# Kernel optimization log

Measured on AMD Instinct MI355X. Metric: run time of the kernel, lower is better.

Reference implementation:

```python
import jax, jax.numpy as jnp
import numpy as np
from jax import lax

EPS = 1e-5  # torch BatchNorm default eps

# Binarization with straight-through estimator (hard-tanh gradient window),
# matching BinaryFunc in dizcza/MCMC_BinaryNet.
@jax.custom_vjp
def binarize(x):
    return jnp.sign(x)

def _bin_fwd(x):
    return jnp.sign(x), x

def _bin_bwd(res, g):
    return (g * (jnp.abs(res) <= 1.0).astype(g.dtype),)

binarize.defvjp(_bin_fwd, _bin_bwd)

def bn2d(x, gamma, beta):
    # training-mode BatchNorm2d: batch stats over (N,H,W), biased variance
    m = x.mean(axis=(0, 2, 3), keepdims=True)
    v = x.var(axis=(0, 2, 3), keepdims=True)
    xn = (x - m) * lax.rsqrt(v + EPS)
    return xn * gamma[None, :, None, None] + beta[None, :, None, None]

def bn1d(x, gamma, beta):
    m = x.mean(axis=0, keepdims=True)
    v = x.var(axis=0, keepdims=True)
    return (x - m) * lax.rsqrt(v + EPS) * gamma[None, :] + beta[None, :]

def bconv(x, w):
    # BinaryDecorator(Conv2d): sign(x) conv sign(W), padding=0, no bias
    return lax.conv_general_dilated(binarize(x), binarize(w), (1, 1), 'VALID',
                                    dimension_numbers=('NCHW', 'OIHW', 'NCHW'))

def maxpool2(x):
    return lax.reduce_window(x, -jnp.inf, lax.max, (1, 1, 2, 2), (1, 1, 2, 2), 'VALID')

def prelu(x, a):
    return jnp.where(x >= 0, x, a * x)


def setup_inputs() -> dict:
    key = jax.random.key(0)
    ks = iter(jax.random.split(key, 16))
    conv_channels = [3, 128, 256, 512]
    fc_sizes = [512 * 6 * 6, 1024, 10]
    d = {'x': jax.random.normal(next(ks), (128, 3, 64, 64), jnp.float32)}
    for i, (cin, cout) in enumerate(zip(conv_channels[:-1], conv_channels[1:])):
        d[f'cg{i}'] = jnp.ones((cin,), jnp.float32)          # BN2d gamma
        d[f'cb{i}'] = jnp.zeros((cin,), jnp.float32)         # BN2d beta
        d[f'cw{i}'] = jax.random.normal(next(ks), (cout, cin, 3, 3), jnp.float32) * 0.05
        d[f'cp{i}'] = jnp.full((1,), 0.25, jnp.float32)      # PReLU (num_parameters=1)
    for i, (fin, fout) in enumerate(zip(fc_sizes[:-1], fc_sizes[1:])):
        d[f'fg{i}'] = jnp.ones((fin,), jnp.float32)
        d[f'fb{i}'] = jnp.zeros((fin,), jnp.float32)
        d[f'fw{i}'] = jax.random.normal(next(ks), (fout, fin), jnp.float32) * 0.05
        d[f'fp{i}'] = jnp.full((1,), 0.25, jnp.float32)
    d['scale'] = jnp.full((1,), 1e-3, jnp.float32)           # ScaleLayer init
    return d


def reference(x, cg0, cb0, cw0, cp0, cg1, cb1, cw1, cp1, cg2, cb2, cw2, cp2,
              fg0, fb0, fw0, fp0, fg1, fb1, fw1, fp1, scale):
    for cg, cb, cw, cp in ((cg0, cb0, cw0, cp0), (cg1, cb1, cw1, cp1), (cg2, cb2, cw2, cp2)):
        x = bn2d(x, cg, cb)
        x = bconv(x, cw)
        x = maxpool2(x)
        x = prelu(x, cp)
    x = x.reshape(x.shape[0], -1)  # [B, 512*6*6]
    for fg, fb, fw, fp in ((fg0, fb0, fw0, fp0), (fg1, fb1, fw1, fp1)):
        x = bn1d(x, fg, fb)
        x = binarize(x) @ binarize(fw).T  # BinaryDecorator(Linear), no bias
        x = prelu(x, fp)
    return x * scale
```

## Files before the change

### kernel.cpp

```cpp
#include <hip/hip_runtime.h>
#include <cstdint>
#include <cstddef>

#define BN_EPS 1e-5


__global__ void zero_d(double* p, int n) {
  int i = blockIdx.x * blockDim.x + threadIdx.x;
  if (i < n) p[i] = 0.0;
}

__global__ void reduce_plane_p(const float* __restrict__ x, double* __restrict__ pp,
                               int C, int HW) {
  int c = blockIdx.x, n = blockIdx.y;
  const float* p = x + ((long)n * C + c) * HW;
  double s = 0.0, s2 = 0.0;
  for (int i = threadIdx.x; i < HW; i += blockDim.x) {
    double v = (double)p[i];
    s += v; s2 += v * v;
  }
  for (int o = 32; o > 0; o >>= 1) {
    s  += __shfl_down(s, o, 64);
    s2 += __shfl_down(s2, o, 64);
  }
  __shared__ double ls[4], ls2[4];
  int lane = threadIdx.x & 63, w = threadIdx.x >> 6;
  if (lane == 0) { ls[w] = s; ls2[w] = s2; }
  __syncthreads();
  if (threadIdx.x == 0) {
    double a = 0, b = 0;
    for (int i = 0; i < 4; i++) { a += ls[i]; b += ls2[i]; }
    long o = ((long)n * C + c) * 2;
    pp[o] = a; pp[o + 1] = b;
  }
}

__global__ void finalize_plane_par(const double* __restrict__ pp, double2* __restrict__ st,
                                   int C, int N, double cnt) {
  int c = blockIdx.x;
  double s = 0.0, s2 = 0.0;
  for (int n = threadIdx.x; n < N; n += blockDim.x) {
    long o = ((long)n * C + c) * 2;
    s  += pp[o];
    s2 += pp[o + 1];
  }
  for (int o = 32; o > 0; o >>= 1) {
    s  += __shfl_down(s, o, 64);
    s2 += __shfl_down(s2, o, 64);
  }
  __shared__ double ls[2], ls2[2];
  int lane = threadIdx.x & 63, w = threadIdx.x >> 6;
  if (lane == 0) { ls[w] = s; ls2[w] = s2; }
  __syncthreads();
  if (threadIdx.x == 0) {
    double a = ls[0] + ls[1], b = ls2[0] + ls2[1];
    double m = a / cnt;
    double v = b / cnt - m * m;
    st[c] = make_double2(m, 1.0 / sqrt(v + BN_EPS));
  }
}

__global__ void finalize_pp1(const double2* __restrict__ pp, double2* __restrict__ st,
                             int C, int Y, double cnt) {
  int c = blockIdx.x;
  double s = 0.0, s2 = 0.0;
  for (int y = threadIdx.x; y < Y; y += blockDim.x) {
    double2 p = pp[(long)y * C + c];
    s += p.x; s2 += p.y;
  }
  for (int o = 32; o > 0; o >>= 1) {
    s  += __shfl_down(s, o, 64);
    s2 += __shfl_down(s2, o, 64);
  }
  __shared__ double ls[4], ls2[4];
  int lane = threadIdx.x & 63, w = threadIdx.x >> 6;
  if (lane == 0) { ls[w] = s; ls2[w] = s2; }
  __syncthreads();
  if (threadIdx.x == 0) {
    double a = ls[0] + ls[1] + ls[2] + ls[3];
    double b = ls2[0] + ls2[1] + ls2[2] + ls2[3];
    double m = a / cnt;
    double v = b / cnt - m * m;
    st[c] = make_double2(m, 1.0 / sqrt(v + BN_EPS));
  }
}

__global__ void finalize_pp2(const double2* __restrict__ pp, double2* __restrict__ st,
                             double cnt) {
  int c = blockIdx.x;
  int cg = c >> 6, l = c & 63;
  double s = 0.0, s2 = 0.0;
  for (int y = threadIdx.x; y < 512; y += blockDim.x) {
    int n = y >> 2, ch = y & 3;
    double2 p = pp[(long)(n * 16 + cg * 4 + ch) * 64 + l];
    s += p.x; s2 += p.y;
  }
  for (int o = 32; o > 0; o >>= 1) {
    s  += __shfl_down(s, o, 64);
    s2 += __shfl_down(s2, o, 64);
  }
  __shared__ double ls[4], ls2[4];
  int lane = threadIdx.x & 63, w = threadIdx.x >> 6;
  if (lane == 0) { ls[w] = s; ls2[w] = s2; }
  __syncthreads();
  if (threadIdx.x == 0) {
    double a = ls[0] + ls[1] + ls[2] + ls[3];
    double b = ls2[0] + ls2[1] + ls2[2] + ls2[3];
    double m = a / cnt;
    double v = b / cnt - m * m;
    st[c] = make_double2(m, 1.0 / sqrt(v + BN_EPS));
  }
}

__global__ void reduce_cols2_i16(const short* __restrict__ x, const float* __restrict__ cp,
                                 double* __restrict__ sums, int R, int F, int RS) {
  int f = blockIdx.x * blockDim.x + threadIdx.x;
  int r0 = blockIdx.y * RS, r1 = min(r0 + RS, R);
  float alpha = cp[0];
  double s = 0.0, s2 = 0.0;
  for (int r = r0; r < r1; r++) {
    int xi = x[(long)r * F + f];
    float pr = xi >= 0 ? (float)xi : alpha * (float)xi;
    double v = (double)pr;
    s += v; s2 += v * v;
  }
  atomicAdd(&sums[2 * f], s);
  atomicAdd(&sums[2 * f + 1], s2);
}

__global__ void reduce_cols2(const float* __restrict__ x, double* __restrict__ sums,
                             int R, int F, int RS) {
  int f = blockIdx.x * blockDim.x + threadIdx.x;
  int r0 = blockIdx.y * RS, r1 = min(r0 + RS, R);
  double s = 0.0, s2 = 0.0;
  for (int r = r0; r < r1; r++) {
    double v = (double)x[(long)r * F + f];
    s += v; s2 += v * v;
  }
  atomicAdd(&sums[2 * f], s);
  atomicAdd(&sums[2 * f + 1], s2);
}

__global__ void finalize_stats(const double* __restrict__ sums, double2* __restrict__ st,
                               int C, double cnt) {
  int c = blockIdx.x * blockDim.x + threadIdx.x;
  if (c >= C) return;
  double m = sums[2 * c] / cnt;
  double v = sums[2 * c + 1] / cnt - m * m;
  st[c] = make_double2(m, 1.0 / sqrt(v + BN_EPS));
}


__global__ void pack_bits_c1(const float* __restrict__ x, const double2* __restrict__ st,
                             const float* __restrict__ g, const float* __restrict__ b,
                             uint64_t* __restrict__ rows, int nwid) {
  long base = ((long)blockIdx.x * 4 + (threadIdx.x >> 6)) * 8;
  int lane = threadIdx.x & 63;
  for (int j = 0; j < 8; j++) {
    long wid = base + j;
    if (wid >= nwid) return;
    int n = (int)(wid / 192), rem = (int)(wid % 192);
    int ci = rem >> 6, y = rem & 63;
    double2 s = st[ci];
    float xv = x[(((long)n * 3 + ci) * 64 + y) * 64 + lane];
    float xn = (float)(((double)xv - s.x) * s.y) * g[ci] + b[ci];
    uint64_t m = __ballot(xn > 0.f);
    if (lane == 0) rows[wid] = m;
  }
}

__global__ void pack_wc1(const float* __restrict__ w, uint32_t* __restrict__ wm) {
  int co = threadIdx.x;
  uint32_t m = 0;
  for (int j = 0; j < 27; j++) m |= (uint32_t)(w[co * 27 + j] > 0.f) << j;
  wm[co] = m;
}

__global__ void pack_cl_i8(const signed char* __restrict__ acl, const double2* __restrict__ st,
                           const float* __restrict__ g, const float* __restrict__ b,
                           const float* __restrict__ cp, uint64_t* __restrict__ out,
                           int C, long nwords, int lw) {
  long base = ((long)blockIdx.x * 4 + (threadIdx.x >> 6)) * 8;
  int lane = threadIdx.x & 63;
  float alpha = cp[0];
  for (int j = 0; j < 8; j++) {
    long wid = base + j;
    if (wid >= nwords) return;
    long row = wid >> lw;
    int w = (int)(wid & ((1 << lw) - 1));
    int c = w * 64 + lane;
    double2 s = st[c];
    int xi = acl[row * C + c];
    float pr = xi >= 0 ? (float)xi : alpha * (float)xi;
    float xn = (float)(((double)pr - s.x) * s.y) * g[c] + b[c];
    uint64_t m = __ballot(xn > 0.f);
    if (lane == 0) out[wid] = m;
  }
}

__global__ void pack_cl_i16(const short* __restrict__ acl, const double2* __restrict__ st,
                            const float* __restrict__ g, const float* __restrict__ b,
                            const float* __restrict__ cp, uint64_t* __restrict__ out,
                            int C, long nwords, int lw) {
  long base = ((long)blockIdx.x * 4 + (threadIdx.x >> 6)) * 8;
  int lane = threadIdx.x & 63;
  float alpha = cp[0];
  for (int j = 0; j < 8; j++) {
    long wid = base + j;
    if (wid >= nwords) return;
    long row = wid >> lw;
    int w = (int)(wid & ((1 << lw) - 1));
    int c = w * 64 + lane;
    double2 s = st[c];
    int xi = acl[row * C + c];
    float pr = xi >= 0 ? (float)xi : alpha * (float)xi;
    float xn = (float)(((double)pr - s.x) * s.y) * g[c] + b[c];
    uint64_t m = __ballot(xn > 0.f);
    if (lane == 0) out[wid] = m;
  }
}

__global__ void pack_wconv(const float* __restrict__ w, uint64_t* __restrict__ out,
                           int CO, int CI, int W) {
  int i = blockIdx.x * blockDim.x + threadIdx.x;
  int total = CO * 9 * W;
  if (i >= total) return;
  int wd = i % W;
  int t = i / W;
  int tap = t % 9, co = t / 9;
  uint64_t bits = 0;
  for (int k = 0; k < 64; k++) {
    int ci = wd * 64 + k;
    bits |= (uint64_t)(w[((long)co * CI + ci) * 9 + tap] > 0.f) << k;
  }
  out[i] = bits;
}

__global__ void pack_nz_i16(const short* __restrict__ x, const double2* __restrict__ st,
                            const float* __restrict__ g, const float* __restrict__ b,
                            const float* __restrict__ cp, uint64_t* __restrict__ out,
                            int R, int F) {
  int Wf = F >> 6;
  long base = ((long)blockIdx.x * 4 + (threadIdx.x >> 6)) * 8;
  int lane = threadIdx.x & 63;
  float alpha = cp[0];
  for (int j = 0; j < 8; j++) {
    long wid = base + j;
    if (wid >= (long)R * Wf) return;
    long r = wid / Wf;
    int w = (int)(wid % Wf);
    int f = w * 64 + lane;
    double2 s = st[f];
    int xi = x[r * F + f];
    float pr = xi >= 0 ? (float)xi : alpha * (float)xi;
    double d = (double)pr - s.x;
    float xn = (float)(d * s.y) * g[f] + b[f];
    uint64_t sm = __ballot(xn > 0.f);
    uint64_t nm = __ballot(d != 0.0);
    if (lane == 0) { out[2 * wid] = sm; out[2 * wid + 1] = nm; }
  }
}

__global__ void pack_nz(const float* __restrict__ x, const double2* __restrict__ st,
                        const float* __restrict__ g, const float* __restrict__ b,
                        uint64_t* __restrict__ out, int R, int F) {
  int Wf = F >> 6;
  long base = ((long)blockIdx.x * 4 + (threadIdx.x >> 6)) * 8;
  int lane = threadIdx.x & 63;
  for (int j = 0; j < 8; j++) {
    long wid = base + j;
    if (wid >= (long)R * Wf) return;
    long r = wid / Wf;
    int w = (int)(wid % Wf);
    int f = w * 64 + lane;
    double2 s = st[f];
    double d = (double)x[r * F + f] - s.x;
    float xn = (float)(d * s.y) * g[f] + b[f];
    uint64_t sm = __ballot(xn > 0.f);
    uint64_t nm = __ballot(d != 0.0);
    if (lane == 0) { out[2 * wid] = sm; out[2 * wid + 1] = nm; }
  }
}

__global__ void pack_wfc2_t(const float* __restrict__ w, uint64_t* __restrict__ out,
                            int O, int F) {
  int Wf = F >> 6;
  long base = ((long)blockIdx.x * 4 + (threadIdx.x >> 6)) * 8;
  int lane = threadIdx.x & 63;
  for (int j = 0; j < 8; j++) {
    long wid = base + j;
    if (wid >= (long)O * Wf) return;
    long o = wid / Wf;
    int wd = (int)(wid % Wf);
    uint64_t m = __ballot(w[o * F + wd * 64 + lane] > 0.f);
    if (lane == 0) out[(long)wd * O + o] = m;
  }
}


__global__ __launch_bounds__(256) void conv1_pool3_i8(const uint64_t* __restrict__ rows,
                                                      const uint32_t* __restrict__ wm,
                                                      const float* __restrict__ cp,
                                                      signed char* __restrict__ out,
                                                      double2* __restrict__ pp) {
  __shared__ uint64_t rL[192];
  __shared__ uint32_t wL[128];
  __shared__ uint32_t mL[61 * 4];
  __shared__ double2 sm[256];
  int n = blockIdx.y, chunk = blockIdx.x, t = threadIdx.x;
  if (t < 192) rL[t] = rows[n * 192 + t];
  if (t < 128) wL[t] = wm[t];
  __syncthreads();
  if (t < 244) {
    int pl = t >> 2, quad = t & 3;
    int pos = chunk * 61 + pl;
    if (pos < 961) {
      int py = pos / 31, px = pos - py * 31;
      int cy = 2 * py + (quad >> 1), cx = 2 * px + (quad & 1);
      uint32_t m = 0;
#pragma unroll
      for (int ci = 0; ci < 3; ci++)
#pragma unroll
        for (int ky = 0; ky < 3; ky++)
          m |= (uint32_t)((rL[ci * 64 + cy + ky] >> cx) & 7) << (ci * 9 + ky * 3);
      mL[pl * 4 + quad] = m;
    }
  }
  __syncthreads();
  int co = t & 127, slot = t >> 7;
  float alpha = cp[0];
  uint32_t w = wL[co];
  double s = 0.0, s2 = 0.0;
  for (int i = slot; i < 61; i += 2) {
    int pos = chunk * 61 + i;
    if (pos >= 961) break;
    int p0 = __popc(mL[4 * i] ^ w);
    int p1 = __popc(mL[4 * i + 1] ^ w);
    int p2 = __popc(mL[4 * i + 2] ^ w);
    int p3 = __popc(mL[4 * i + 3] ^ w);
    int dot = 27 - 2 * min(min(p0, p1), min(p2, p3));
    out[((long)n * 961 + pos) * 128 + co] = (signed char)dot;
    float pr = dot >= 0 ? (float)dot : alpha * (float)dot;
    double v = (double)pr;
    s += v; s2 += v * v;
  }
  sm[t] = make_double2(s, s2);
  __syncthreads();
  if (t < 128) {
    double2 a = sm[t], b = sm[t + 128];
    pp[((long)n * 16 + chunk) * 128 + t] = make_double2(a.x + b.x, a.y + b.y);
  }
}

template <int W, int IH, int PH, int CHUNK>
__global__ __attribute__((amdgpu_flat_work_group_size(256, 256),
                          amdgpu_waves_per_eu(3, 4)))
void convp_carry_i16(const uint64_t* __restrict__ in, const uint64_t* __restrict__ wt,
                     const float* __restrict__ cp, short* __restrict__ out,
                     double2* __restrict__ pp, int CO) {
  __shared__ uint64_t sIn[10 * IH * W];
  __shared__ double2 sm[256];
  int n = blockIdx.y;
  int cg = blockIdx.x / CHUNK, chunk = blockIdx.x % CHUNK;
  int t = threadIdx.x, lane = t & 63, slot = t >> 6;
  int r0 = chunk * 8;
  int nr = min(10, IH - r0);
  const uint64_t* src = in + ((long)n * IH + r0) * (IH * W);
  for (int i = t; i < nr * IH * W; i += 256) sIn[i] = src[i];
  int co = cg * 64 + lane;
  uint64_t wr[9 * W];
  const uint64_t* wg = wt + (long)co * (9 * W);
#pragma unroll
  for (int i = 0; i < 9 * W; i++) wr[i] = wg[i];
  __syncthreads();
  int py = chunk * 4 + slot;
  float alpha = cp[0];
  double s = 0.0, s2 = 0.0;
  if (py < PH) {
    const int K = 9 * 64 * W;
    const uint64_t* base = &sIn[(2 * slot) * (IH * W)];
    uint64_t c[4][2 * W];
#pragma unroll
    for (int cy = 0; cy < 4; cy++) {
      const uint64_t* p = &base[(cy * IH) * W];
#pragma unroll
      for (int j = 0; j < 2 * W; j++) c[cy][j] = p[j];
    }
#pragma unroll
    for (int px = 0; px < PH; px++) {
      int a00 = 0, a01 = 0, a10 = 0, a11 = 0;
#pragma unroll
      for (int cy = 0; cy < 4; cy++) {
        uint64_t f[2 * W];
        const uint64_t* fp = &base[(cy * IH + 2 * px + 2) * W];
#pragma unroll
        for (int j = 0; j < 2 * W; j++) f[j] = fp[j];
#pragma unroll
        for (int col = 0; col < 4; col++) {
#pragma unroll
          for (int wd = 0; wd < W; wd++) {
            uint64_t v = (col < 2) ? c[cy][col * W + wd] : f[(col - 2) * W + wd];
#pragma unroll
            for (int dy = 0; dy < 2; dy++) {
              int ky = cy - dy;
              if (ky < 0 || ky > 2) continue;
#pragma unroll
              for (int dx = 0; dx < 2; dx++) {
                int kx = col - dx;
                if (kx < 0 || kx > 2) continue;
                int p = __popcll(v ^ wr[(ky * 3 + kx) * W + wd]);
                if (dy == 0) { if (dx == 0) a00 += p; else a01 += p; }
                else         { if (dx == 0) a10 += p; else a11 += p; }
              }
            }
          }
        }
#pragma unroll
        for (int j = 0; j < 2 * W; j++) c[cy][j] = f[j];
      }
      int dot = K - 2 * min(min(a00, a01), min(a10, a11));
      out[((long)n * PH * PH + py * PH + px) * CO + co] = (short)dot;
      float pr = dot >= 0 ? (float)dot : alpha * (float)dot;
      double v = (double)pr;
      s += v; s2 += v * v;
    }
  }
  sm[t] = make_double2(s, s2);
  __syncthreads();
  if (t < 64) {
    double2 a = sm[t], b = sm[64 + t], cc = sm[128 + t], d = sm[192 + t];
    pp[((long)blockIdx.y * 16 + blockIdx.x) * 64 + t] =
        make_double2(a.x + b.x + cc.x + d.x, a.y + b.y + cc.y + d.y);
  }
}

#define TAP2(acc, P, wa, wb) acc += __popcll((P).x ^ (wa)) + __popcll((P).y ^ (wb));
#define ROWT(aL, aR, pA, pB, pC, pD, WX, WY, WZ)                \
  TAP2(aL, pA, WX.x, WX.y) TAP2(aL, pB, WY.x, WY.y)             \
  TAP2(aL, pC, WZ.x, WZ.y)                                      \
  TAP2(aR, pB, WX.x, WX.y) TAP2(aR, pC, WY.x, WY.y)             \
  TAP2(aR, pD, WZ.x, WZ.y)

__global__ __attribute__((amdgpu_flat_work_group_size(256, 256),
                          amdgpu_waves_per_eu(4, 6)))
void convs3_i16(const uint64_t* __restrict__ in, const uint64_t* __restrict__ wt,
                short* __restrict__ out) {
  __shared__ uint64_t sIn[14 * 14 * 4];
  int n = blockIdx.y, cg = blockIdx.x;
  int t = threadIdx.x, lane = t & 63, slot = t >> 6;
  const uint64_t* src = in + (long)n * 784;
  for (int i = t; i < 784; i += 256) sIn[i] = src[i];
  int h = lane >> 5;
  int co = cg * 32 + (lane & 31);
  const uint64_t* wg = wt + co * 36 + 2 * h;
  ulonglong2 W0 = *(const ulonglong2*)(wg + 0);
  ulonglong2 W1 = *(const ulonglong2*)(wg + 4);
  ulonglong2 W2 = *(const ulonglong2*)(wg + 8);
  ulonglong2 W3 = *(const ulonglong2*)(wg + 12);
  ulonglong2 W4 = *(const ulonglong2*)(wg + 16);
  ulonglong2 W5 = *(const ulonglong2*)(wg + 20);
  ulonglong2 W6 = *(const ulonglong2*)(wg + 24);
  ulonglong2 W7 = *(const ulonglong2*)(wg + 28);
  ulonglong2 W8 = *(const ulonglong2*)(wg + 32);
  __syncthreads();
  short* outb = out + ((long)n * 512 + co) * 36;
#pragma unroll
  for (int k = 0; k < 9; k++) {
    int pos = slot + 4 * k;
    int py = pos / 6, px = pos - py * 6;
    const uint64_t* q = sIn + ((2 * py) * 14 + 2 * px) * 4 + 2 * h;
    int a00 = 0, a01 = 0, a10 = 0, a11 = 0;
    {
      ulonglong2 p0 = *(const ulonglong2*)(q + 0);
      ulonglong2 p1 = *(const ulonglong2*)(q + 4);
      ulonglong2 p2 = *(const ulonglong2*)(q + 8);
      ulonglong2 p3 = *(const ulonglong2*)(q + 12);
      ROWT(a00, a01, p0, p1, p2, p3, W0, W1, W2)
    }
    {
      const uint64_t* q1 = q + 56;
      ulonglong2 p0 = *(const ulonglong2*)(q1 + 0);
      ulonglong2 p1 = *(const ulonglong2*)(q1 + 4);
      ulonglong2 p2 = *(const ulonglong2*)(q1 + 8);
      ulonglong2 p3 = *(const ulonglong2*)(q1 + 12);
      ROWT(a00, a01, p0, p1, p2, p3, W3, W4, W5)
      ROWT(a10, a11, p0, p1, p2, p3, W0, W1, W2)
    }
    {
      const uint64_t* q2 = q + 112;
      ulonglong2 p0 = *(const ulonglong2*)(q2 + 0);
      ulonglong2 p1 = *(const ulonglong2*)(q2 + 4);
      ulonglong2 p2 = *(const ulonglong2*)(q2 + 8);
      ulonglong2 p3 = *(const ulonglong2*)(q2 + 12);
      ROWT(a00, a01, p0, p1, p2, p3, W6, W7, W8)
      ROWT(a10, a11, p0, p1, p2, p3, W3, W4, W5)
    }
    {
      const uint64_t* q3 = q + 168;
      ulonglong2 p0 = *(const ulonglong2*)(q3 + 0);
      ulonglong2 p1 = *(const ulonglong2*)(q3 + 4);
      ulonglong2 p2 = *(const ulonglong2*)(q3 + 8);
      ulonglong2 p3 = *(const ulonglong2*)(q3 + 12);
      ROWT(a10, a11, p0, p1, p2, p3, W6, W7, W8)
    }
    int t00 = a00 + __shfl_xor(a00, 32);
    int t01 = a01 + __shfl_xor(a01, 32);
    int t10 = a10 + __shfl_xor(a10, 32);
    int t11 = a11 + __shfl_xor(a11, 32);
    if (h == 0) {
      int dot = 2304 - 2 * min(min(t00, t01), min(t10, t11));
      outb[pos] = (short)dot;
    }
  }
}


__global__ void fc_bin2(const uint64_t* __restrict__ xp, const uint64_t* __restrict__ wp_t,
                        const float* __restrict__ cp, float* __restrict__ out,
                        int O, int Wf) {
  __shared__ uint64_t xs[2][288], xz[2][288];
  int r0 = blockIdx.y * 2;
  for (int i = threadIdx.x; i < 2 * Wf; i += blockDim.x) {
    int rr = i / Wf, wd = i - rr * Wf;
    xs[rr][wd] = xp[(((long)(r0 + rr)) * Wf + wd) * 2];
    xz[rr][wd] = xp[(((long)(r0 + rr)) * Wf + wd) * 2 + 1];
  }
  __syncthreads();
  int o = blockIdx.x * blockDim.x + threadIdx.x;
  if (o >= O) return;
  int pc0 = 0, pc1 = 0, nz0 = 0, nz1 = 0;
  for (int wd = 0; wd < Wf; wd++) {
    uint64_t w = wp_t[(long)wd * O + o];
    uint64_t z0 = xz[0][wd], z1 = xz[1][wd];
    pc0 += __popcll((xs[0][wd] ^ w) & z0);
    pc1 += __popcll((xs[1][wd] ^ w) & z1);
    nz0 += __popcll(z0);
    nz1 += __popcll(z1);
  }
  float alpha = cp[0];
  int d0 = nz0 - 2 * pc0, d1 = nz1 - 2 * pc1;
  float f0 = (float)d0, f1 = (float)d1;
  out[(long)r0 * O + o] = d0 >= 0 ? f0 : alpha * f0;
  out[(long)(r0 + 1) * O + o] = d1 >= 0 ? f1 : alpha * f1;
}

__global__ void fc_bin_scale(const uint64_t* __restrict__ xp, const uint64_t* __restrict__ wp_t,
                             const float* __restrict__ cp, const float* __restrict__ scale,
                             float* __restrict__ out, int R, int O, int Wf) {
  int i = blockIdx.x * blockDim.x + threadIdx.x;
  if (i >= R * O) return;
  int o = i % O, r = i / O;
  int pc = 0, nzc = 0;
  for (int wd = 0; wd < Wf; wd++) {
    uint64_t nz = xp[((long)r * Wf + wd) * 2 + 1];
    pc += __popcll((xp[((long)r * Wf + wd) * 2] ^ wp_t[(long)wd * O + o]) & nz);
    nzc += __popcll(nz);
  }
  int dot = nzc - 2 * pc;
  float f = (float)dot;
  float alpha = cp[0];
  f = dot >= 0 ? f : alpha * f;
  out[i] = f * scale[0];
}


extern "C" void kernel_launch(void* const* d_in, const int* in_sizes, int n_in,
                              void* d_out, int out_size, void* d_ws, size_t ws_size,
                              hipStream_t stream) {
  const float* x   = (const float*)d_in[0];
  const float* cg0 = (const float*)d_in[1];
  const float* cb0 = (const float*)d_in[2];
  const float* cw0 = (const float*)d_in[3];
  const float* cp0 = (const float*)d_in[4];
  const float* cg1 = (const float*)d_in[5];
  const float* cb1 = (const float*)d_in[6];
  const float* cw1 = (const float*)d_in[7];
  const float* cp1 = (const float*)d_in[8];
  const float* cg2 = (const float*)d_in[9];
  const float* cb2 = (const float*)d_in[10];
  const float* cw2 = (const float*)d_in[11];
  const float* cp2 = (const float*)d_in[12];
  const float* fg0 = (const float*)d_in[13];
  const float* fb0 = (const float*)d_in[14];
  const float* fw0 = (const float*)d_in[15];
  const float* fp0 = (const float*)d_in[16];
  const float* fg1 = (const float*)d_in[17];
  const float* fb1 = (const float*)d_in[18];
  const float* fw1 = (const float*)d_in[19];
  const float* fp1 = (const float*)d_in[20];
  const float* scl = (const float*)d_in[21];

  char* ws = (char*)d_ws;
  size_t off = 0;
  auto alloc = [&](size_t bytes) {
    size_t r = off;
    off += (bytes + 255) & ~(size_t)255;
    return r;
  };
  const int C0_OFF = 0, C1_OFF = 16, C2_OFF = 160, C3_OFF = 448, C4_OFF = 18944;
  const int NCH = 19968;

  double*   sums  = (double*)(ws + alloc((size_t)NCH * 2 * sizeof(double)));
  double2*  stats = (double2*)(ws + alloc((size_t)NCH * sizeof(double2)));
  double*   pplane= (double*)(ws + alloc(128L * 3 * 2 * sizeof(double)));
  double2*  pp1   = (double2*)(ws + alloc(2048L * 128 * sizeof(double2)));
  double2*  pp2   = (double2*)(ws + alloc(2048L * 64 * sizeof(double2)));
  uint64_t* rows0 = (uint64_t*)(ws + alloc(128L * 3 * 64 * 8));
  uint32_t* wm1   = (uint32_t*)(ws + alloc(128L * 4));
  signed char* a1 = (signed char*)(ws + alloc(128L * 961 * 128));
  uint64_t* s1p   = (uint64_t*)(ws + alloc(128L * 961 * 2 * 8));
  uint64_t* w1p   = (uint64_t*)(ws + alloc(256L * 9 * 2 * 8));
  short*    a2    = (short*)(ws + alloc(128L * 196 * 256 * 2));
  uint64_t* s2p   = (uint64_t*)(ws + alloc(128L * 196 * 4 * 8));
  uint64_t* w2p   = (uint64_t*)(ws + alloc(512L * 9 * 4 * 8));
  short*    a3    = (short*)(ws + alloc(128L * 512 * 36 * 2));
  uint64_t* s3p   = (uint64_t*)(ws + alloc(128L * 288 * 2 * 8));
  uint64_t* w3p   = (uint64_t*)(ws + alloc(1024L * 288 * 8));
  float*    f1    = (float*)(ws + alloc(128L * 1024 * 4));
  uint64_t* s4p   = (uint64_t*)(ws + alloc(128L * 16 * 2 * 8));
  uint64_t* w4p   = (uint64_t*)(ws + alloc(10L * 16 * 8));

  const int B = 256;

  zero_d<<<dim3(153), B, 0, stream>>>(sums + 2 * C3_OFF, (NCH - C3_OFF) * 2);

  reduce_plane_p<<<dim3(3, 128), B, 0, stream>>>(x, pplane, 3, 4096);
  finalize_plane_par<<<dim3(3), 128, 0, stream>>>(pplane, stats + C0_OFF, 3, 128, 524288.0);
  pack_bits_c1<<<dim3(768), B, 0, stream>>>(x, stats + C0_OFF, cg0, cb0, rows0, 24576);
  pack_wc1<<<1, 128, 0, stream>>>(cw0, wm1);
  conv1_pool3_i8<<<dim3(16, 128), B, 0, stream>>>(rows0, wm1, cp0, a1, pp1);

  finalize_pp1<<<dim3(128), B, 0, stream>>>(pp1, stats + C1_OFF, 128, 2048, 123008.0);
  pack_cl_i8<<<dim3(7688), B, 0, stream>>>(a1, stats + C1_OFF, cg1, cb1, cp0, s1p, 128, 246016L, 1);
  pack_wconv<<<dim3(18), B, 0, stream>>>(cw1, w1p, 256, 128, 2);
  convp_carry_i16<2, 31, 14, 4><<<dim3(16, 128), B, 0, stream>>>(s1p, w1p, cp1, a2, pp2, 256);

  finalize_pp2<<<dim3(256), B, 0, stream>>>(pp2, stats + C2_OFF, 25088.0);
  pack_cl_i16<<<dim3(3136), B, 0, stream>>>(a2, stats + C2_OFF, cg2, cb2, cp1, s2p, 256, 100352L, 2);
  pack_wconv<<<dim3(72), B, 0, stream>>>(cw2, w2p, 512, 256, 4);
  convs3_i16<<<dim3(16, 128), B, 0, stream>>>(s2p, w2p, a3);

  reduce_cols2_i16<<<dim3(72, 8), B, 0, stream>>>(a3, cp2, sums + 2 * C3_OFF, 128, 18432, 16);
  finalize_stats<<<dim3(72), B, 0, stream>>>(sums + 2 * C3_OFF, stats + C3_OFF, 18432, 128.0);
  pack_nz_i16<<<dim3(1152), B, 0, stream>>>(a3, stats + C3_OFF, fg0, fb0, cp2, s3p, 128, 18432);
  pack_wfc2_t<<<dim3(9216), B, 0, stream>>>(fw0, w3p, 1024, 18432);
  fc_bin2<<<dim3(4, 64), B, 0, stream>>>(s3p, w3p, fp0, f1, 1024, 288);

  reduce_cols2<<<dim3(4, 8), B, 0, stream>>>(f1, sums + 2 * C4_OFF, 128, 1024, 16);
  finalize_stats<<<dim3(4), B, 0, stream>>>(sums + 2 * C4_OFF, stats + C4_OFF, 1024, 128.0);
  pack_nz<<<dim3(64), B, 0, stream>>>(f1, stats + C4_OFF, fg1, fb1, s4p, 128, 1024);
  pack_wfc2_t<<<dim3(5), B, 0, stream>>>(fw1, w4p, 10, 1024);
  fc_bin_scale<<<dim3(5), B, 0, stream>>>(s4p, w4p, fp1, scl, (float*)d_out, 128, 10, 16);
}
```

Baseline: 494.7 us.

## Merge weight packing into one launch and fuse BN stat finalization into consumers

All weight-binarization kernels and the zeroing of the sums buffer are merged into a single multi-role launch. The BN statistic finalize kernels are folded into the packing kernels that consume them: layer-0 stats are computed in shared memory inside pack_bits_c1, and FC0 stats are computed on the fly from the sums. The FC0 GEMM now emits per-row-pair partial sums, so the last BN, pack and FC1 run in one fused per-row kernel. This removes about ten kernel launches and their serialization gaps, at the cost of redundant per-block stat recomputation.

```diff
diff --git a/kernel.cpp b/kernel.cpp
--- a/kernel.cpp
+++ b/kernel.cpp
@@ -5,9 +5,61 @@
 #define BN_EPS 1e-5
 
 
-__global__ void zero_d(double* p, int n) {
-  int i = blockIdx.x * blockDim.x + threadIdx.x;
-  if (i < n) p[i] = 0.0;
+__global__ void pack_weights_all(const float* __restrict__ cw0, const float* __restrict__ cw1,
+                                 const float* __restrict__ cw2, const float* __restrict__ fw0,
+                                 const float* __restrict__ fw1,
+                                 uint32_t* __restrict__ wm1, uint64_t* __restrict__ w1p,
+                                 uint64_t* __restrict__ w2p, uint64_t* __restrict__ w3p,
+                                 uint64_t* __restrict__ w4p, double* __restrict__ zp, int zn) {
+  int bb = blockIdx.x, t = threadIdx.x, lane = t & 63, wv = t >> 6;
+  if (bb == 0) {
+    if (t < 128) {
+      uint32_t m = 0;
+      for (int j = 0; j < 27; j++) m |= (uint32_t)(cw0[t * 27 + j] > 0.f) << j;
+      wm1[t] = m;
+    }
+  } else if (bb < 19) {
+    int i = (bb - 1) * 256 + t;
+    if (i < 4608) {
+      int wd = i % 2, t2 = i / 2, tap = t2 % 9, co = t2 / 9;
+      uint64_t bits = 0;
+      for (int k = 0; k < 64; k++)
+        bits |= (uint64_t)(cw1[((long)co * 128 + wd * 64 + k) * 9 + tap] > 0.f) << k;
+      w1p[i] = bits;
+    }
+  } else if (bb < 91) {
+    int i = (bb - 19) * 256 + t;
+    if (i < 18432) {
+      int wd = i % 4, t2 = i / 4, tap = t2 % 9, co = t2 / 9;
+      uint64_t bits = 0;
+      for (int k = 0; k < 64; k++)
+        bits |= (uint64_t)(cw2[((long)co * 256 + wd * 64 + k) * 9 + tap] > 0.f) << k;
+      w2p[i] = bits;
+    }
+  } else if (bb < 9307) {
+    long base = ((long)(bb - 91) * 4 + wv) * 8;
+    for (int j = 0; j < 8; j++) {
+      long wid = base + j;
+      if (wid >= 294912) break;
+      long o = wid / 288;
+      int wd = (int)(wid % 288);
+      uint64_t m = __ballot(fw0[o * 18432 + wd * 64 + lane] > 0.f);
+      if (lane == 0) w3p[(long)wd * 1024 + o] = m;
+    }
+  } else if (bb < 9312) {
+    long base = ((long)(bb - 9307) * 4 + wv) * 8;
+    for (int j = 0; j < 8; j++) {
+      long wid = base + j;
+      if (wid >= 160) break;
+      long o = wid / 16;
+      int wd = (int)(wid % 16);
+      uint64_t m = __ballot(fw1[o * 1024 + wd * 64 + lane] > 0.f);
+      if (lane == 0) w4p[(long)wd * 10 + o] = m;
+    }
+  } else {
+    int i = (bb - 9312) * 256 + t;
+    if (i < zn) zp[i] = 0.0;
+  }
 }
 
 __global__ void reduce_plane_p(const float* __restrict__ x, double* __restrict__ pp,
@@ -35,28 +87,37 @@
   }
 }
 
-__global__ void finalize_plane_par(const double* __restrict__ pp, double2* __restrict__ st,
-                                   int C, int N, double cnt) {
-  int c = blockIdx.x;
-  double s = 0.0, s2 = 0.0;
-  for (int n = threadIdx.x; n < N; n += blockDim.x) {
-    long o = ((long)n * C + c) * 2;
-    s  += pp[o];
-    s2 += pp[o + 1];
-  }
-  for (int o = 32; o > 0; o >>= 1) {
-    s  += __shfl_down(s, o, 64);
-    s2 += __shfl_down(s2, o, 64);
-  }
-  __shared__ double ls[2], ls2[2];
-  int lane = threadIdx.x & 63, w = threadIdx.x >> 6;
-  if (lane == 0) { ls[w] = s; ls2[w] = s2; }
-  __syncthreads();
-  if (threadIdx.x == 0) {
-    double a = ls[0] + ls[1], b = ls2[0] + ls2[1];
-    double m = a / cnt;
-    double v = b / cnt - m * m;
-    st[c] = make_double2(m, 1.0 / sqrt(v + BN_EPS));
+__global__ void pack_bits_c1_f(const float* __restrict__ x, const double* __restrict__ pplane,
+                               const float* __restrict__ g, const float* __restrict__ b,
+                               uint64_t* __restrict__ rows, int nwid) {
+  __shared__ double2 stc[3];
+  int t = threadIdx.x, lane = t & 63, wv = t >> 6;
+  if (wv < 3) {
+    int c = wv;
+    double s  = pplane[((long)lane * 3 + c) * 2]     + pplane[((long)(lane + 64) * 3 + c) * 2];
+    double s2 = pplane[((long)lane * 3 + c) * 2 + 1] + pplane[((long)(lane + 64) * 3 + c) * 2 + 1];
+    for (int o = 32; o > 0; o >>= 1) {
+      s  += __shfl_down(s, o, 64);
+      s2 += __shfl_down(s2, o, 64);
+    }
+    if (lane == 0) {
+      double m = s / 524288.0;
+      double v = s2 / 524288.0 - m * m;
+      stc[c] = make_double2(m, 1.0 / sqrt(v + BN_EPS));
+    }
+  }
+  __syncthreads();
+  long base = ((long)blockIdx.x * 4 + wv) * 8;
+  for (int j = 0; j < 8; j++) {
+    long wid = base + j;
+    if (wid >= nwid) return;
+    int n = (int)(wid / 192), rem = (int)(wid % 192);
+    int ci = rem >> 6, y = rem & 63;
+    double2 s = stc[ci];
+    float xv = x[(((long)n * 3 + ci) * 64 + y) * 64 + lane];
+    float xn = (float)(((double)xv - s.x) * s.y) * g[ci] + b[ci];
+    uint64_t m = __ballot(xn > 0.f);
+    if (lane == 0) rows[wid] = m;
   }
 }
 
@@ -128,53 +189,6 @@
   atomicAdd(&sums[2 * f + 1], s2);
 }
 
-__global__ void reduce_cols2(const float* __restrict__ x, double* __restrict__ sums,
-                             int R, int F, int RS) {
-  int f = blockIdx.x * blockDim.x + threadIdx.x;
-  int r0 = blockIdx.y * RS, r1 = min(r0 + RS, R);
-  double s = 0.0, s2 = 0.0;
-  for (int r = r0; r < r1; r++) {
-    double v = (double)x[(long)r * F + f];
-    s += v; s2 += v * v;
-  }
-  atomicAdd(&sums[2 * f], s);
-  atomicAdd(&sums[2 * f + 1], s2);
-}
-
-__global__ void finalize_stats(const double* __restrict__ sums, double2* __restrict__ st,
-                               int C, double cnt) {
-  int c = blockIdx.x * blockDim.x + threadIdx.x;
-  if (c >= C) return;
-  double m = sums[2 * c] / cnt;
-  double v = sums[2 * c + 1] / cnt - m * m;
-  st[c] = make_double2(m, 1.0 / sqrt(v + BN_EPS));
-}
-
-
-__global__ void pack_bits_c1(const float* __restrict__ x, const double2* __restrict__ st,
-                             const float* __restrict__ g, const float* __restrict__ b,
-                             uint64_t* __restrict__ rows, int nwid) {
-  long base = ((long)blockIdx.x * 4 + (threadIdx.x >> 6)) * 8;
-  int lane = threadIdx.x & 63;
-  for (int j = 0; j < 8; j++) {
-    long wid = base + j;
-    if (wid >= nwid) return;
-    int n = (int)(wid / 192), rem = (int)(wid % 192);
-    int ci = rem >> 6, y = rem & 63;
-    double2 s = st[ci];
-    float xv = x[(((long)n * 3 + ci) * 64 + y) * 64 + lane];
-    float xn = (float)(((double)xv - s.x) * s.y) * g[ci] + b[ci];
-    uint64_t m = __ballot(xn > 0.f);
-    if (lane == 0) rows[wid] = m;
-  }
-}
-
-__global__ void pack_wc1(const float* __restrict__ w, uint32_t* __restrict__ wm) {
-  int co = threadIdx.x;
-  uint32_t m = 0;
-  for (int j = 0; j < 27; j++) m |= (uint32_t)(w[co * 27 + j] > 0.f) << j;
-  wm[co] = m;
-}
 
 __global__ void pack_cl_i8(const signed char* __restrict__ acl, const double2* __restrict__ st,
                            const float* __restrict__ g, const float* __restrict__ b,
@@ -220,26 +234,10 @@
   }
 }
 
-__global__ void pack_wconv(const float* __restrict__ w, uint64_t* __restrict__ out,
-                           int CO, int CI, int W) {
-  int i = blockIdx.x * blockDim.x + threadIdx.x;
-  int total = CO * 9 * W;
-  if (i >= total) return;
-  int wd = i % W;
-  int t = i / W;
-  int tap = t % 9, co = t / 9;
-  uint64_t bits = 0;
-  for (int k = 0; k < 64; k++) {
-    int ci = wd * 64 + k;
-    bits |= (uint64_t)(w[((long)co * CI + ci) * 9 + tap] > 0.f) << k;
-  }
-  out[i] = bits;
-}
-
-__global__ void pack_nz_i16(const short* __restrict__ x, const double2* __restrict__ st,
-                            const float* __restrict__ g, const float* __restrict__ b,
-                            const float* __restrict__ cp, uint64_t* __restrict__ out,
-                            int R, int F) {
+__global__ void pack_nz_st_i16(const short* __restrict__ x, const double* __restrict__ sums,
+                               const float* __restrict__ g, const float* __restrict__ b,
+                               const float* __restrict__ cp, uint64_t* __restrict__ out,
+                               int R, int F) {
   int Wf = F >> 6;
   long base = ((long)blockIdx.x * 4 + (threadIdx.x >> 6)) * 8;
   int lane = threadIdx.x & 63;
@@ -250,50 +248,16 @@
     long r = wid / Wf;
     int w = (int)(wid % Wf);
     int f = w * 64 + lane;
-    double2 s = st[f];
+    double m = sums[2 * f] / 128.0;
+    double v = sums[2 * f + 1] / 128.0 - m * m;
+    double rs = 1.0 / sqrt(v + BN_EPS);
     int xi = x[r * F + f];
     float pr = xi >= 0 ? (float)xi : alpha * (float)xi;
-    double d = (double)pr - s.x;
-    float xn = (float)(d * s.y) * g[f] + b[f];
+    double d = (double)pr - m;
+    float xn = (float)(d * rs) * g[f] + b[f];
     uint64_t sm = __ballot(xn > 0.f);
     uint64_t nm = __ballot(d != 0.0);
     if (lane == 0) { out[2 * wid] = sm; out[2 * wid + 1] = nm; }
-  }
-}
-
-__global__ void pack_nz(const float* __restrict__ x, const double2* __restrict__ st,
-                        const float* __restrict__ g, const float* __restrict__ b,
-                        uint64_t* __restrict__ out, int R, int F) {
-  int Wf = F >> 6;
-  long base = ((long)blockIdx.x * 4 + (threadIdx.x >> 6)) * 8;
-  int lane = threadIdx.x & 63;
-  for (int j = 0; j < 8; j++) {
-    long wid = base + j;
-    if (wid >= (long)R * Wf) return;
-    long r = wid / Wf;
-    int w = (int)(wid % Wf);
-    int f = w * 64 + lane;
-    double2 s = st[f];
-    double d = (double)x[r * F + f] - s.x;
-    float xn = (float)(d * s.y) * g[f] + b[f];
-    uint64_t sm = __ballot(xn > 0.f);
-    uint64_t nm = __ballot(d != 0.0);
-    if (lane == 0) { out[2 * wid] = sm; out[2 * wid + 1] = nm; }
-  }
-}
-
-__global__ void pack_wfc2_t(const float* __restrict__ w, uint64_t* __restrict__ out,
-                            int O, int F) {
-  int Wf = F >> 6;
-  long base = ((long)blockIdx.x * 4 + (threadIdx.x >> 6)) * 8;
-  int lane = threadIdx.x & 63;
-  for (int j = 0; j < 8; j++) {
-    long wid = base + j;
-    if (wid >= (long)O * Wf) return;
-    long o = wid / Wf;
-    int wd = (int)(wid % Wf);
-    uint64_t m = __ballot(w[o * F + wd * 64 + lane] > 0.f);
-    if (lane == 0) out[(long)wd * O + o] = m;
   }
 }
 
@@ -515,9 +479,9 @@
 }
 
 
-__global__ void fc_bin2(const uint64_t* __restrict__ xp, const uint64_t* __restrict__ wp_t,
-                        const float* __restrict__ cp, float* __restrict__ out,
-                        int O, int Wf) {
+__global__ void fc_bin2_pp(const uint64_t* __restrict__ xp, const uint64_t* __restrict__ wp_t,
+                           const float* __restrict__ cp, float* __restrict__ out,
+                           double2* __restrict__ pp3, int O, int Wf) {
   __shared__ uint64_t xs[2][288], xz[2][288];
   int r0 = blockIdx.y * 2;
   for (int i = threadIdx.x; i < 2 * Wf; i += blockDim.x) {
@@ -539,28 +503,51 @@
   }
   float alpha = cp[0];
   int d0 = nz0 - 2 * pc0, d1 = nz1 - 2 * pc1;
-  float f0 = (float)d0, f1 = (float)d1;
-  out[(long)r0 * O + o] = d0 >= 0 ? f0 : alpha * f0;
-  out[(long)(r0 + 1) * O + o] = d1 >= 0 ? f1 : alpha * f1;
-}
-
-__global__ void fc_bin_scale(const uint64_t* __restrict__ xp, const uint64_t* __restrict__ wp_t,
-                             const float* __restrict__ cp, const float* __restrict__ scale,
-                             float* __restrict__ out, int R, int O, int Wf) {
-  int i = blockIdx.x * blockDim.x + threadIdx.x;
-  if (i >= R * O) return;
-  int o = i % O, r = i / O;
-  int pc = 0, nzc = 0;
-  for (int wd = 0; wd < Wf; wd++) {
-    uint64_t nz = xp[((long)r * Wf + wd) * 2 + 1];
-    pc += __popcll((xp[((long)r * Wf + wd) * 2] ^ wp_t[(long)wd * O + o]) & nz);
-    nzc += __popcll(nz);
-  }
-  int dot = nzc - 2 * pc;
-  float f = (float)dot;
-  float alpha = cp[0];
-  f = dot >= 0 ? f : alpha * f;
-  out[i] = f * scale[0];
+  float v0 = (float)d0, v1 = (float)d1;
+  v0 = d0 >= 0 ? v0 : alpha * v0;
+  v1 = d1 >= 0 ? v1 : alpha * v1;
+  out[(long)r0 * O + o] = v0;
+  out[(long)(r0 + 1) * O + o] = v1;
+  double dv0 = (double)v0, dv1 = (double)v1;
+  pp3[(long)blockIdx.y * O + o] = make_double2(dv0 + dv1, dv0 * dv0 + dv1 * dv1);
+}
+
+__global__ void fc1_fused(const float* __restrict__ f1, const double2* __restrict__ pp3,
+                          const float* __restrict__ g, const float* __restrict__ b,
+                          const uint64_t* __restrict__ w4p, const float* __restrict__ cp,
+                          const float* __restrict__ scale, float* __restrict__ out) {
+  __shared__ uint64_t xs[16], xz[16];
+  int r = blockIdx.x, t = threadIdx.x, lane = t & 63, wv = t >> 6;
+  for (int it = 0; it < 4; it++) {
+    int f = it * 256 + t;
+    double s = 0.0, s2 = 0.0;
+    for (int y = 0; y < 64; y++) {
+      double2 p = pp3[(long)y * 1024 + f];
+      s += p.x; s2 += p.y;
+    }
+    double m = s / 128.0;
+    double v = s2 / 128.0 - m * m;
+    double rs = 1.0 / sqrt(v + BN_EPS);
+    double d = (double)f1[(long)r * 1024 + f] - m;
+    float xn = (float)(d * rs) * g[f] + b[f];
+    uint64_t smk = __ballot(xn > 0.f);
+    uint64_t nmk = __ballot(d != 0.0);
+    if (lane == 0) { xs[it * 4 + wv] = smk; xz[it * 4 + wv] = nmk; }
+  }
+  __syncthreads();
+  if (t < 10) {
+    int pc = 0, nzc = 0;
+    for (int wd = 0; wd < 16; wd++) {
+      uint64_t nz = xz[wd];
+      pc += __popcll((xs[wd] ^ w4p[wd * 10 + t]) & nz);
+      nzc += __popcll(nz);
+    }
+    int dot = nzc - 2 * pc;
+    float f = (float)dot;
+    float alpha = cp[0];
+    f = dot >= 0 ? f : alpha * f;
+    out[(long)r * 10 + t] = f * scale[0];
+  }
 }
 
 
@@ -597,14 +584,14 @@
     off += (bytes + 255) & ~(size_t)255;
     return r;
   };
-  const int C0_OFF = 0, C1_OFF = 16, C2_OFF = 160, C3_OFF = 448, C4_OFF = 18944;
-  const int NCH = 19968;
-
-  double*   sums  = (double*)(ws + alloc((size_t)NCH * 2 * sizeof(double)));
-  double2*  stats = (double2*)(ws + alloc((size_t)NCH * sizeof(double2)));
+  const int C1_OFF = 16, C2_OFF = 160;
+
+  double*   sums  = (double*)(ws + alloc(18432L * 2 * sizeof(double)));
+  double2*  stats = (double2*)(ws + alloc(512L * sizeof(double2)));
   double*   pplane= (double*)(ws + alloc(128L * 3 * 2 * sizeof(double)));
   double2*  pp1   = (double2*)(ws + alloc(2048L * 128 * sizeof(double2)));
   double2*  pp2   = (double2*)(ws + alloc(2048L * 64 * sizeof(double2)));
+  double2*  pp3   = (double2*)(ws + alloc(64L * 1024 * sizeof(double2)));
   uint64_t* rows0 = (uint64_t*)(ws + alloc(128L * 3 * 64 * 8));
   uint32_t* wm1   = (uint32_t*)(ws + alloc(128L * 4));
   signed char* a1 = (signed char*)(ws + alloc(128L * 961 * 128));
@@ -617,38 +604,29 @@
   uint64_t* s3p   = (uint64_t*)(ws + alloc(128L * 288 * 2 * 8));
   uint64_t* w3p   = (uint64_t*)(ws + alloc(1024L * 288 * 8));
   float*    f1    = (float*)(ws + alloc(128L * 1024 * 4));
-  uint64_t* s4p   = (uint64_t*)(ws + alloc(128L * 16 * 2 * 8));
   uint64_t* w4p   = (uint64_t*)(ws + alloc(10L * 16 * 8));
 
   const int B = 256;
 
-  zero_d<<<dim3(153), B, 0, stream>>>(sums + 2 * C3_OFF, (NCH - C3_OFF) * 2);
+  pack_weights_all<<<dim3(9456), B, 0, stream>>>(cw0, cw1, cw2, fw0, fw1,
+                                                 wm1, w1p, w2p, w3p, w4p,
+                                                 sums, 36864);
 
   reduce_plane_p<<<dim3(3, 128), B, 0, stream>>>(x, pplane, 3, 4096);
-  finalize_plane_par<<<dim3(3), 128, 0, stream>>>(pplane, stats + C0_OFF, 3, 128, 524288.0);
-  pack_bits_c1<<<dim3(768), B, 0, stream>>>(x, stats + C0_OFF, cg0, cb0, rows0, 24576);
-  pack_wc1<<<1, 128, 0, stream>>>(cw0, wm1);
+  pack_bits_c1_f<<<dim3(768), B, 0, stream>>>(x, pplane, cg0, cb0, rows0, 24576);
   conv1_pool3_i8<<<dim3(16, 128), B, 0, stream>>>(rows0, wm1, cp0, a1, pp1);
 
   finalize_pp1<<<dim3(128), B, 0, stream>>>(pp1, stats + C1_OFF, 128, 2048, 123008.0);
   pack_cl_i8<<<dim3(7688), B, 0, stream>>>(a1, stats + C1_OFF, cg1, cb1, cp0, s1p, 128, 246016L, 1);
-  pack_wconv<<<dim3(18), B, 0, stream>>>(cw1, w1p, 256, 128, 2);
   convp_carry_i16<2, 31, 14, 4><<<dim3(16, 128), B, 0, stream>>>(s1p, w1p, cp1, a2, pp2, 256);
 
   finalize_pp2<<<dim3(256), B, 0, stream>>>(pp2, stats + C2_OFF, 25088.0);
   pack_cl_i16<<<dim3(3136), B, 0, stream>>>(a2, stats + C2_OFF, cg2, cb2, cp1, s2p, 256, 100352L, 2);
-  pack_wconv<<<dim3(72), B, 0, stream>>>(cw2, w2p, 512, 256, 4);
   convs3_i16<<<dim3(16, 128), B, 0, stream>>>(s2p, w2p, a3);
 
-  reduce_cols2_i16<<<dim3(72, 8), B, 0, stream>>>(a3, cp2, sums + 2 * C3_OFF, 128, 18432, 16);
-  finalize_stats<<<dim3(72), B, 0, stream>>>(sums + 2 * C3_OFF, stats + C3_OFF, 18432, 128.0);
-  pack_nz_i16<<<dim3(1152), B, 0, stream>>>(a3, stats + C3_OFF, fg0, fb0, cp2, s3p, 128, 18432);
-  pack_wfc2_t<<<dim3(9216), B, 0, stream>>>(fw0, w3p, 1024, 18432);
-  fc_bin2<<<dim3(4, 64), B, 0, stream>>>(s3p, w3p, fp0, f1, 1024, 288);
-
-  reduce_cols2<<<dim3(4, 8), B, 0, stream>>>(f1, sums + 2 * C4_OFF, 128, 1024, 16);
-  finalize_stats<<<dim3(4), B, 0, stream>>>(sums + 2 * C4_OFF, stats + C4_OFF, 1024, 128.0);
-  pack_nz<<<dim3(64), B, 0, stream>>>(f1, stats + C4_OFF, fg1, fb1, s4p, 128, 1024);
-  pack_wfc2_t<<<dim3(5), B, 0, stream>>>(fw1, w4p, 10, 1024);
-  fc_bin_scale<<<dim3(5), B, 0, stream>>>(s4p, w4p, fp1, scl, (float*)d_out, 128, 10, 16);
-}
+  reduce_cols2_i16<<<dim3(72, 8), B, 0, stream>>>(a3, cp2, sums, 128, 18432, 16);
+  pack_nz_st_i16<<<dim3(1152), B, 0, stream>>>(a3, sums, fg0, fb0, cp2, s3p, 128, 18432);
+  fc_bin2_pp<<<dim3(4, 64), B, 0, stream>>>(s3p, w3p, fp0, f1, pp3, 1024, 288);
+
+  fc1_fused<<<dim3(128), B, 0, stream>>>(f1, pp3, fg1, fb1, w4p, fp1, scl, (float*)d_out);
+}
```

New measurement: 455.3 us. -8.0%, faster.
